# Kernel optimization log

Measured on AMD Instinct MI355X. Metric: run time of the kernel, lower is better.

Reference implementation:

```python
import jax, jax.numpy as jnp
import numpy as np

N_NODES = 400
HID = 96
DEC = 64
FEAT_STATIC = 8
FEAT = FEAT_STATIC + N_NODES  # 408
EPS = 1e-8


def prelu(x, a):
    # single-parameter PReLU (torch default num_parameters=1)
    return jnp.where(x >= 0, x, a * x)


def setup_inputs() -> dict:
    key = jax.random.key(0)
    ks = jax.random.split(key, 16)
    B = 16
    E = N_NODES * (N_NODES - 1) // 2  # 79800

    x = jax.random.normal(ks[0], (B, E), dtype=jnp.float32)
    node_features = jax.random.normal(ks[1], (B, N_NODES, FEAT_STATIC), dtype=jnp.float32)
    sc_matrix = jax.random.uniform(ks[2], (B, N_NODES, N_NODES), dtype=jnp.float32)

    # normalization buffers (computed from train split in torch; random stand-ins)
    static_mean = jax.random.normal(ks[3], (1, 1, FEAT_STATIC), dtype=jnp.float32) * 0.1
    static_std = jnp.ones((1, 1, FEAT_STATIC), dtype=jnp.float32)

    def lin(k, fin, fout):
        kw, kb = jax.random.split(k)
        lim = 1.0 / np.sqrt(fin)
        W = jax.random.uniform(kw, (fin, fout), minval=-lim, maxval=lim, dtype=jnp.float32)
        b = jax.random.uniform(kb, (fout,), minval=-lim, maxval=lim, dtype=jnp.float32)
        return W, b

    W_e1, b_e1 = lin(ks[4], FEAT, HID)
    W_e2, b_e2 = lin(ks[5], HID, HID)
    W_d1, b_d1 = lin(ks[6], 3 * HID, DEC)  # symmetric decoder: 3 * node_embed_dim
    W_d2, b_d2 = lin(ks[7], DEC, DEC)
    W_d3, b_d3 = lin(ks[8], DEC, 1)

    a25 = jnp.float32(0.25)

    ei_np, ej_np = np.triu_indices(N_NODES, k=1)
    ei = jnp.asarray(ei_np, dtype=jnp.int32)
    ej = jnp.asarray(ej_np, dtype=jnp.int32)

    return {
        "x": x, "node_features": node_features, "sc_matrix": sc_matrix,
        "static_mean": static_mean, "static_std": static_std,
        "W_e1": W_e1, "b_e1": b_e1, "a_e1": a25,
        "W_e2": W_e2, "b_e2": b_e2, "a_e2": a25,
        "W_d1": W_d1, "b_d1": b_d1, "a_d1": a25,
        "W_d2": W_d2, "b_d2": b_d2, "a_d2": a25,
        "W_d3": W_d3, "b_d3": b_d3,
        "ei": ei, "ej": ej,
    }


def reference(x, node_features, sc_matrix, static_mean, static_std,
              W_e1, b_e1, a_e1, W_e2, b_e2, a_e2,
              W_d1, b_d1, a_d1, W_d2, b_d2, a_d2, W_d3, b_d3, ei, ej):
    # x (SC upper triangle) is only used for batch size in the torch module.
    # static anatomical block: z-score with train stats
    s = (node_features - static_mean) / (static_std + EPS)  # [B,N,8]
    # sc_row block, 'brain_scale': divide by per-matrix mean
    m = sc_matrix / jnp.maximum(
        jnp.mean(sc_matrix, axis=(-2, -1), keepdims=True), EPS)  # [B,N,N]
    feats = jnp.concatenate([s, m], axis=-1)  # [B,N,408]

    # shared node encoder (dropout inactive at eval)
    h = prelu(feats @ W_e1 + b_e1, a_e1)
    h = prelu(h @ W_e2 + b_e2, a_e2)  # [B,N,96]

    # per-edge gather over upper-triangle indices
    h_i = h[:, ei, :]  # [B,E,96]
    h_j = h[:, ej, :]
    # symmetric edge features
    edge_feat = jnp.concatenate(
        [h_i + h_j, jnp.abs(h_i - h_j), h_i * h_j], axis=-1)  # [B,E,288]

    z = prelu(edge_feat @ W_d1 + b_d1, a_d1)
    z = prelu(z @ W_d2 + b_d2, a_d2)
    out = (z @ W_d3 + b_d3)[..., 0]  # [B,E]
    return out
```

## Files before the change

kernel.cpp:

```cpp
#include <hip/hip_runtime.h>

#define NN 400
#define HID 96
#define EDGES 79800
#define BATCH 16
#define ROWS (BATCH*EDGES)
#define NTILES 4988
#define NBLK 768

typedef _Float16 f16;
typedef f16 f16x2 __attribute__((ext_vector_type(2)));
typedef f16 f16x8 __attribute__((ext_vector_type(8)));
typedef __fp16 fp16x2 __attribute__((ext_vector_type(2)));
typedef float f32x16 __attribute__((ext_vector_type(16)));
typedef unsigned int u32;
typedef unsigned long long u64;

union H8 { f16x8 h; u32 u[4]; f16x2 p[4]; fp16x2 q[4]; u64 d[2]; };
union C2 { f16x2 h; fp16x2 q; u32 u; };

__device__ inline f16x2 pkrtz(float a, float b) {
  C2 c; c.q = __builtin_amdgcn_cvt_pkrtz(a, b); return c.h;
}
__device__ inline u32 pkrtz_u(float a, float b) {
  C2 c; c.q = __builtin_amdgcn_cvt_pkrtz(a, b); return c.u;
}
__device__ inline float fdot2a(f16x2 a, f16x2 b, float c) {
#if __has_builtin(__builtin_amdgcn_fdot2)
  C2 ca, cb; ca.h = a; cb.h = b;
  return __builtin_amdgcn_fdot2(ca.q, cb.q, c, false);
#else
  return c + (float)a.x*(float)b.x + (float)a.y*(float)b.y;
#endif
}

__device__ inline f16x8 habs8(f16x8 x) {
  H8 t; t.h = x;
  t.u[0] &= 0x7fff7fffu; t.u[1] &= 0x7fff7fffu;
  t.u[2] &= 0x7fff7fffu; t.u[3] &= 0x7fff7fffu;
  return t.h;
}

__device__ inline f16x8 pack8(float a0,float a1,float a2,float a3,
                              float a4,float a5,float a6,float a7){
  H8 u;
  u.p[0] = pkrtz(a0,a1);
  u.p[1] = pkrtz(a2,a3);
  u.p[2] = pkrtz(a4,a5);
  u.p[3] = pkrtz(a6,a7);
  return u.h;
}

__global__ void prep_mean_kernel(const float* __restrict__ We1, const float* __restrict__ We2,
                                 const float* __restrict__ W1, const float* __restrict__ W2,
                                 const float* __restrict__ sc,
                                 u32* __restrict__ wq, float* __restrict__ mpart) {
  if (blockIdx.x >= 140) {
    int p = blockIdx.x - 140;
    int b = p >> 2, part = p & 3;
    const float4* src = (const float4*)(sc + (size_t)b*160000) + part*10000;
    float s = 0.f;
    for (int i = threadIdx.x; i < 10000; i += 256) {
      float4 v = src[i];
      s += (v.x + v.y) + (v.z + v.w);
    }
    __shared__ float red[256];
    red[threadIdx.x] = s; __syncthreads();
    for (int off = 128; off > 0; off >>= 1) {
      if (threadIdx.x < off) red[threadIdx.x] += red[threadIdx.x + off];
      __syncthreads();
    }
    if (threadIdx.x == 0) mpart[p] = red[0];
    return;
  }
  int D = blockIdx.x*256 + threadIdx.x;
  float v0, v1;
  if (D < 9216) {
    int frag = D >> 8;  int t = frag >> 1, q = frag & 1;
    int rem = D & 255;  int lane = rem >> 2, dj = rem & 3;
    int c = lane & 31, h2 = lane >> 5;
    int k = 16*t + 8*h2 + 2*dj;
    int d = 32*q + c;
    v0 = W1[k*64 + d]; v1 = W1[(k+1)*64 + d];
  } else if (D < 11264) {
    int Dl = D - 9216;
    int frag = Dl >> 8; int t2 = frag >> 1, q = frag & 1;
    int rem = Dl & 255; int lane = rem >> 2, dj = rem & 3;
    int c = lane & 31, h2 = lane >> 5;
    int p = 8*t2 + 4*h2 + dj;
    int d = 32*q + c;
    v0 = W2[p*64 + d]; v1 = W2[(p+32)*64 + d];
  } else if (D < 31232) {
    int Dl = D - 11264;
    int frag = Dl >> 8; int t = frag/3, ct = frag - 3*t;
    int rem = Dl & 255; int lane = rem >> 2, dj = rem & 3;
    int c = lane & 31, h2 = lane >> 5;
    int k0 = 16*t + 8*h2 + 2*dj, k1 = k0 + 1;
    int d = 32*ct + c;
    v0 = (k0 < 400) ? We1[(8+k0)*96 + d] : (k0 < 408 ? We1[(k0-400)*96 + d] : 0.f);
    v1 = (k1 < 400) ? We1[(8+k1)*96 + d] : (k1 < 408 ? We1[(k1-400)*96 + d] : 0.f);
  } else {
    int Dl = D - 31232;
    int frag = Dl >> 8; int t = frag/3, ct = frag - 3*t;
    int rem = Dl & 255; int lane = rem >> 2, dj = rem & 3;
    int c = lane & 31, h2 = lane >> 5;
    int k = 16*t + 8*h2 + 2*dj;
    int p0 = (k   < 64) ? ((k&1)*32 + (k>>1))       : k;
    int p1 = (k+1 < 64) ? (((k+1)&1)*32 + ((k+1)>>1)) : (k+1);
    int d = 32*ct + c;
    v0 = We2[p0*96 + d]; v1 = We2[p1*96 + d];
  }
  wq[D] = pkrtz_u(v0, v1);
}

#define EST 210
__global__ __launch_bounds__(64) void enc_kernel(
    const float* __restrict__ sc, const float* __restrict__ nf,
    const float* __restrict__ smean, const float* __restrict__ sstd,
    const float* __restrict__ be1, const float* __restrict__ ae1,
    const float* __restrict__ be2, const float* __restrict__ ae2,
    const float* __restrict__ mpart, const u32* __restrict__ wq,
    f16* __restrict__ hout) {
  __shared__ u32 st[32*EST];
  const int lane = threadIdx.x;
  const int rt = blockIdx.x;
  const int r0 = rt*32;
  {
    int row = lane >> 1, half = lane & 1;
    int r = r0 + row;
    int b = r / 400;
    float ms = mpart[4*b] + mpart[4*b+1] + mpart[4*b+2] + mpart[4*b+3];
    float rm = 1.f / fmaxf(ms*(1.f/160000.f), 1e-8f);
    const float4* src = (const float4*)(sc + (size_t)r*400) + half*50;
    u32* dst = st + row*EST + half*100;
#pragma unroll 5
    for (int i = 0; i < 50; ++i) {
      float4 v = src[i];
      u32 lo = pkrtz_u(v.x*rm, v.y*rm);
      u32 hi = pkrtz_u(v.z*rm, v.w*rm);
      u64 w = (u64)lo | ((u64)hi << 32);
      *(u64*)(dst + 2*i) = w;
    }
  }
  const int c = lane & 31, h2 = lane >> 5;
  const float a1 = *ae1, a2 = *ae2;
  f32x16 acc[3];
#pragma unroll
  for (int q = 0; q < 3; ++q) {
    float bv = be1[32*q + c];
#pragma unroll
    for (int i = 0; i < 16; ++i) acc[q][i] = bv;
  }
  const u32* wb1 = wq + 11264;
#pragma unroll 5
  for (int t = 0; t < 25; ++t) {
    H8 av;
    const u32* ap = st + c*EST + 8*t + 4*h2;
    av.d[0] = *(const u64*)ap;
    av.d[1] = *(const u64*)(ap + 2);
#pragma unroll
    for (int ct = 0; ct < 3; ++ct) {
      f16x8 bf = *(const f16x8*)(wb1 + ((t*3+ct)*64 + lane)*4);
      acc[ct] = __builtin_amdgcn_mfma_f32_32x32x16_f16(av.h, bf, acc[ct], 0,0,0);
    }
  }
  {
    f16x8 af = {};
    if (h2 == 0) {
      int r = r0 + c;
      float q0[8];
#pragma unroll
      for (int j = 0; j < 8; ++j)
        q0[j] = (nf[r*8 + j] - smean[j]) / (sstd[j] + 1e-8f);
      af = pack8(q0[0],q0[1],q0[2],q0[3],q0[4],q0[5],q0[6],q0[7]);
    }
#pragma unroll
    for (int ct = 0; ct < 3; ++ct) {
      f16x8 bf = *(const f16x8*)(wb1 + ((25*3+ct)*64 + lane)*4);
      acc[ct] = __builtin_amdgcn_mfma_f32_32x32x16_f16(af, bf, acc[ct], 0,0,0);
    }
  }
  u32* zb = st;
#pragma unroll
  for (int r = 0; r < 16; ++r) {
    float x0 = acc[0][r]; x0 = fmaxf(x0, a1*x0);
    float x1 = acc[1][r]; x1 = fmaxf(x1, a1*x1);
    float x2 = acc[2][r]; x2 = fmaxf(x2, a1*x2);
    int row = (r & 3) + 8*(r >> 2) + 4*h2;
    zb[row*52 + c] = pkrtz_u(x0, x1);
    ((f16*)zb)[row*104 + 64 + c] = (f16)x2;
  }
  f32x16 acc2[3];
#pragma unroll
  for (int q = 0; q < 3; ++q) {
    float bv = be2[32*q + c];
#pragma unroll
    for (int i = 0; i < 16; ++i) acc2[q][i] = bv;
  }
  const u32* wb2 = wq + 31232;
#pragma unroll
  for (int t = 0; t < 6; ++t) {
    f16x8 af = *(const f16x8*)((const f16*)zb + c*104 + 16*t + 8*h2);
#pragma unroll
    for (int ct = 0; ct < 3; ++ct) {
      f16x8 bf = *(const f16x8*)(wb2 + ((t*3+ct)*64 + lane)*4);
      acc2[ct] = __builtin_amdgcn_mfma_f32_32x32x16_f16(af, bf, acc2[ct], 0,0,0);
    }
  }
#pragma unroll
  for (int ct = 0; ct < 3; ++ct)
#pragma unroll
    for (int rr = 0; rr < 16; ++rr) {
      int row = (rr & 3) + 8*(rr >> 2) + 4*h2;
      float v = acc2[ct][rr]; v = fmaxf(v, a2*v);
      hout[(r0 + row)*96 + 32*ct + c] = (f16)v;
    }
}

__global__ __launch_bounds__(256, 2) void decoder_kernel(
    const f16* __restrict__ hbuf, const u32* __restrict__ wq,
    const float* __restrict__ b1, const float* __restrict__ b2,
    const float* __restrict__ ad1, const float* __restrict__ ad2,
    const float* __restrict__ W3, const float* __restrict__ b3p,
    const int* __restrict__ ei, const int* __restrict__ ej,
    float* __restrict__ out) {
  __shared__ f16 wfr[17408];
  __shared__ u32 zbuf[4][1152];
  {
    float4* dst = (float4*)wfr;
    const float4* src = (const float4*)wq;
    for (int i = threadIdx.x; i < 2176; i += 256) dst[i] = src[i];
  }
  __syncthreads();
  const int lane = threadIdx.x & 63;
  const int wid  = threadIdx.x >> 6;
  const int c = lane & 31, h2 = lane >> 5;
  u32* zb = zbuf[wid];
  f16x8 bp5[2];
  bp5[0] = *(const f16x8*)(wq + ((34+0)*64 + lane)*4);
  bp5[1] = *(const f16x8*)(wq + ((34+1)*64 + lane)*4);
  f16x8 w2f[4][2];
#pragma unroll
  for (int t2 = 0; t2 < 4; ++t2) {
    w2f[t2][0] = *(const f16x8*)(wq + 9216 + ((t2*2+0)*64 + lane)*4);
    w2f[t2][1] = *(const f16x8*)(wq + 9216 + ((t2*2+1)*64 + lane)*4);
  }
  const float b1x = b1[c], b1y = b1[c+32];
  const float b2x = b2[c], b2y = b2[c+32];
  const float a1 = *ad1, a2 = *ad2, b3 = *b3p;
  const f16x2 a1v = pkrtz(a1, a1);
  const f16x2 a2v = pkrtz(a2, a2);
  const f16x2 w3p = pkrtz(W3[c], W3[c+32]);
  const f16x2 ones2 = pkrtz(1.f, 1.f);

  int tile = blockIdx.x;
  int nii[2], njj[2]; bool nvalid[2];
#pragma unroll
  for (int m = 0; m < 2; ++m) {
    int r = tile*256 + wid*64 + 32*m + c;
    nvalid[m] = (r < ROWS);
    unsigned rr = nvalid[m] ? (unsigned)r : (unsigned)(ROWS-1);
    unsigned bb = rr / (unsigned)EDGES;
    int e = (int)(rr - bb*(unsigned)EDGES);
    nii[m] = (int)(bb*NN) + ei[e];
    njj[m] = (int)(bb*NN) + ej[e];
  }

  for (; tile < NTILES; tile += NBLK) {
    const int rbase = tile*256 + wid*64;
    const f16* pi[2]; const f16* pj[2];
    bool valid[2];
#pragma unroll
    for (int m = 0; m < 2; ++m) {
      valid[m] = nvalid[m];
      pi[m] = hbuf + (nii[m]*HID + 8*h2);
      pj[m] = hbuf + (njj[m]*HID + 8*h2);
    }
    int ntile = tile + NBLK;
    if (ntile < NTILES) {
#pragma unroll
      for (int m = 0; m < 2; ++m) {
        int r = ntile*256 + wid*64 + 32*m + c;
        nvalid[m] = (r < ROWS);
        unsigned rr = nvalid[m] ? (unsigned)r : (unsigned)(ROWS-1);
        unsigned bb = rr / (unsigned)EDGES;
        int e = (int)(rr - bb*(unsigned)EDGES);
        nii[m] = (int)(bb*NN) + ei[e];
        njj[m] = (int)(bb*NN) + ej[e];
      }
    }
    f32x16 acc[2][2];
#pragma unroll
    for (int r = 0; r < 16; ++r) {
      acc[0][0][r] = b1x; acc[0][1][r] = b1y;
      acc[1][0][r] = b1x; acc[1][1][r] = b1y;
    }
#pragma unroll
    for (int t = 0; t < 6; ++t) {
      f16x8 bs0 = *(const f16x8*)(wfr + (((t   )*2+0)*64 + lane)*8);
      f16x8 bs1 = *(const f16x8*)(wfr + (((t   )*2+1)*64 + lane)*8);
      f16x8 bd0 = *(const f16x8*)(wfr + (((t+ 6)*2+0)*64 + lane)*8);
      f16x8 bd1 = *(const f16x8*)(wfr + (((t+ 6)*2+1)*64 + lane)*8);
      f16x8 bp0 = (t < 5) ? *(const f16x8*)(wfr + (((t+12)*2+0)*64 + lane)*8) : bp5[0];
      f16x8 bp1 = (t < 5) ? *(const f16x8*)(wfr + (((t+12)*2+1)*64 + lane)*8) : bp5[1];
#pragma unroll
      for (int m = 0; m < 2; ++m) {
        f16x8 hi = *(const f16x8*)(pi[m] + 16*t);
        f16x8 hj = *(const f16x8*)(pj[m] + 16*t);
        f16x8 su = hi + hj;
        f16x8 di = habs8(hi - hj);
        f16x8 pr = hi * hj;
        acc[m][0] = __builtin_amdgcn_mfma_f32_32x32x16_f16(su, bs0, acc[m][0], 0,0,0);
        acc[m][1] = __builtin_amdgcn_mfma_f32_32x32x16_f16(su, bs1, acc[m][1], 0,0,0);
        acc[m][0] = __builtin_amdgcn_mfma_f32_32x32x16_f16(di, bd0, acc[m][0], 0,0,0);
        acc[m][1] = __builtin_amdgcn_mfma_f32_32x32x16_f16(di, bd1, acc[m][1], 0,0,0);
        acc[m][0] = __builtin_amdgcn_mfma_f32_32x32x16_f16(pr, bp0, acc[m][0], 0,0,0);
        acc[m][1] = __builtin_amdgcn_mfma_f32_32x32x16_f16(pr, bp1, acc[m][1], 0,0,0);
      }
    }
#pragma unroll
    for (int m = 0; m < 2; ++m) {
#pragma unroll
      for (int r = 0; r < 16; ++r) {
        f16x2 p = pkrtz(acc[m][0][r], acc[m][1][r]);
        p = __builtin_elementwise_max(p, p * a1v);
        C2 cv; cv.h = p;
        int row = (r & 3) + 8*(r >> 2) + 4*h2;
        zb[row*36 + c] = cv.u;
      }
      f16x8 za[4];
#pragma unroll
      for (int t2 = 0; t2 < 4; ++t2)
        za[t2] = *(const f16x8*)((const f16*)zb + (c*36 + 8*t2 + 4*h2)*2);
      f32x16 zacc[2];
#pragma unroll
      for (int r = 0; r < 16; ++r) { zacc[0][r] = b2x; zacc[1][r] = b2y; }
#pragma unroll
      for (int t2 = 0; t2 < 4; ++t2) {
        zacc[0] = __builtin_amdgcn_mfma_f32_32x32x16_f16(za[t2], w2f[t2][0], zacc[0], 0,0,0);
        zacc[1] = __builtin_amdgcn_mfma_f32_32x32x16_f16(za[t2], w2f[t2][1], zacc[1], 0,0,0);
      }
#pragma unroll
      for (int r = 0; r < 16; ++r) {
        f16x2 p = pkrtz(zacc[0][r], zacc[1][r]);
        p = __builtin_elementwise_max(p, p * a2v);
        p = p * w3p;
        C2 cv; cv.h = p;
        int row = (r & 3) + 8*(r >> 2) + 4*h2;
        zb[row*36 + c] = cv.u;
      }
      float ssum = 0.f;
#pragma unroll
      for (int g = 0; g < 4; ++g) {
        H8 v; v.h = *(const f16x8*)((const f16*)zb + (c*36 + 16*h2 + 4*g)*2);
#pragma unroll
        for (int dw = 0; dw < 4; ++dw)
          ssum = fdot2a(v.p[dw], ones2, ssum);
      }
      ssum += __shfl_xor(ssum, 32);
      if (h2 == 0 && valid[m]) out[rbase + 32*m + c] = ssum + b3;
    }
  }
}

extern "C" void kernel_launch(void* const* d_in, const int* in_sizes, int n_in,
                              void* d_out, int out_size, void* d_ws, size_t ws_size,
                              hipStream_t stream) {
  const float* nf  = (const float*)d_in[1];
  const float* sc  = (const float*)d_in[2];
  const float* sm  = (const float*)d_in[3];
  const float* ss  = (const float*)d_in[4];
  const float* We1 = (const float*)d_in[5];
  const float* be1 = (const float*)d_in[6];
  const float* ae1 = (const float*)d_in[7];
  const float* We2 = (const float*)d_in[8];
  const float* be2 = (const float*)d_in[9];
  const float* ae2 = (const float*)d_in[10];
  const float* W1  = (const float*)d_in[11];
  const float* b1  = (const float*)d_in[12];
  const float* a1  = (const float*)d_in[13];
  const float* W2  = (const float*)d_in[14];
  const float* b2  = (const float*)d_in[15];
  const float* a2  = (const float*)d_in[16];
  const float* W3  = (const float*)d_in[17];
  const float* b3  = (const float*)d_in[18];
  const int*   ei  = (const int*)d_in[19];
  const int*   ej  = (const int*)d_in[20];
  float* out = (float*)d_out;

  char* ws = (char*)d_ws;
  float* mpart = (float*)ws;
  f16*   hbuf = (f16*)(ws + 256);
  u32*   wq   = (u32*)(ws + 256 + 1228800);

  prep_mean_kernel<<<204, 256, 0, stream>>>(We1, We2, W1, W2, sc, wq, mpart);
  enc_kernel<<<200, 64, 0, stream>>>(sc, nf, sm, ss, be1, ae1, be2, ae2,
                                     mpart, wq, hbuf);
  decoder_kernel<<<NBLK, 256, 0, stream>>>(hbuf, wq, b1, b2, a1, a2, W3, b3,
                                           ei, ej, out);
}
```

Measured before the change: 208.4 us.

## Split encoder K-loop across four waves, widen mean reduction, drop decoder LDS weights

The encoder now runs four waves per block. Each wave handles a slice of the first-layer K loop, and the partial accumulators are reduced through LDS before the second layer, which is split by output column tile across three waves. The sc mean reduction uses 16 parts per matrix instead of 4. The decoder no longer stages first-layer weights in LDS and reads them straight from global memory (cache). The decoder grid also grows from 768 to 1024 blocks. The aim is more parallelism in the small encoder and less LDS pressure and setup in the decoder. The cost is extra global/cache traffic for weight fragments in the decoder's inner loop and extra syncs in the encoder.

After: 212.6 us. 2.0% more time.

```diff
diff --git a/kernel.cpp b/kernel.cpp
--- a/kernel.cpp
+++ b/kernel.cpp
@@ -6,7 +6,7 @@
 #define BATCH 16
 #define ROWS (BATCH*EDGES)
 #define NTILES 4988
-#define NBLK 768
+#define NBLK 1024
 
 typedef _Float16 f16;
 typedef f16 f16x2 __attribute__((ext_vector_type(2)));
@@ -18,6 +18,7 @@
 
 union H8 { f16x8 h; u32 u[4]; f16x2 p[4]; fp16x2 q[4]; u64 d[2]; };
 union C2 { f16x2 h; fp16x2 q; u32 u; };
+union A16 { f32x16 v; float4 f[4]; };
 
 __device__ inline f16x2 pkrtz(float a, float b) {
   C2 c; c.q = __builtin_amdgcn_cvt_pkrtz(a, b); return c.h;
@@ -57,10 +58,10 @@
                                  u32* __restrict__ wq, float* __restrict__ mpart) {
   if (blockIdx.x >= 140) {
     int p = blockIdx.x - 140;
-    int b = p >> 2, part = p & 3;
-    const float4* src = (const float4*)(sc + (size_t)b*160000) + part*10000;
+    int b = p >> 4, part = p & 15;
+    const float4* src = (const float4*)(sc + (size_t)b*160000) + part*2500;
     float s = 0.f;
-    for (int i = threadIdx.x; i < 10000; i += 256) {
+    for (int i = threadIdx.x; i < 2500; i += 256) {
       float4 v = src[i];
       s += (v.x + v.y) + (v.z + v.w);
     }
@@ -105,116 +106,127 @@
     int rem = Dl & 255; int lane = rem >> 2, dj = rem & 3;
     int c = lane & 31, h2 = lane >> 5;
     int k = 16*t + 8*h2 + 2*dj;
-    int p0 = (k   < 64) ? ((k&1)*32 + (k>>1))       : k;
-    int p1 = (k+1 < 64) ? (((k+1)&1)*32 + ((k+1)>>1)) : (k+1);
     int d = 32*ct + c;
-    v0 = We2[p0*96 + d]; v1 = We2[p1*96 + d];
+    v0 = We2[k*96 + d]; v1 = We2[(k+1)*96 + d];
   }
   wq[D] = pkrtz_u(v0, v1);
 }
 
-#define EST 210
-__global__ __launch_bounds__(64) void enc_kernel(
+__global__ __launch_bounds__(256) void enc_kernel(
     const float* __restrict__ sc, const float* __restrict__ nf,
     const float* __restrict__ smean, const float* __restrict__ sstd,
     const float* __restrict__ be1, const float* __restrict__ ae1,
     const float* __restrict__ be2, const float* __restrict__ ae2,
     const float* __restrict__ mpart, const u32* __restrict__ wq,
     f16* __restrict__ hout) {
-  __shared__ u32 st[32*EST];
-  const int lane = threadIdx.x;
-  const int rt = blockIdx.x;
-  const int r0 = rt*32;
+  __shared__ u32 lds[12288 + 1664];
+  const int tid = threadIdx.x;
+  const int wid = tid >> 6, lane = tid & 63;
+  const int c = lane & 31, h2 = lane >> 5;
+  const int r0 = blockIdx.x * 32;
   {
-    int row = lane >> 1, half = lane & 1;
+    int row = tid >> 3, seg = tid & 7;
     int r = r0 + row;
     int b = r / 400;
-    float ms = mpart[4*b] + mpart[4*b+1] + mpart[4*b+2] + mpart[4*b+3];
+    float ms = 0.f;
+    const float4* mp4 = (const float4*)(mpart + 16*b);
+#pragma unroll
+    for (int k = 0; k < 4; ++k) { float4 v = mp4[k]; ms += (v.x+v.y)+(v.z+v.w); }
     float rm = 1.f / fmaxf(ms*(1.f/160000.f), 1e-8f);
-    const float4* src = (const float4*)(sc + (size_t)r*400) + half*50;
-    u32* dst = st + row*EST + half*100;
-#pragma unroll 5
-    for (int i = 0; i < 50; ++i) {
-      float4 v = src[i];
-      u32 lo = pkrtz_u(v.x*rm, v.y*rm);
-      u32 hi = pkrtz_u(v.z*rm, v.w*rm);
-      u64 w = (u64)lo | ((u64)hi << 32);
-      *(u64*)(dst + 2*i) = w;
-    }
-  }
-  const int c = lane & 31, h2 = lane >> 5;
-  const float a1 = *ae1, a2 = *ae2;
-  f32x16 acc[3];
-#pragma unroll
-  for (int q = 0; q < 3; ++q) {
-    float bv = be1[32*q + c];
-#pragma unroll
-    for (int i = 0; i < 16; ++i) acc[q][i] = bv;
-  }
+    const float4* src = (const float4*)(sc + (size_t)r*400);
+#pragma unroll
+    for (int i = 0; i < 13; ++i) {
+      int col4 = seg + 8*i;
+      if (col4 < 100) {
+        float4 v = src[col4];
+        u32 lo = pkrtz_u(v.x*rm, v.y*rm);
+        u32 hi = pkrtz_u(v.z*rm, v.w*rm);
+        *(u64*)(lds + row*210 + col4*2) = (u64)lo | ((u64)hi << 32);
+      }
+    }
+  }
+  __syncthreads();
+  int tb = (wid==0) ? 0 : (wid==1) ? 7 : (wid==2) ? 14 : 20;
+  int te = (wid==0) ? 7 : (wid==1) ? 14 : (wid==2) ? 20 : 26;
+  f32x16 acc[3] = {};
   const u32* wb1 = wq + 11264;
-#pragma unroll 5
-  for (int t = 0; t < 25; ++t) {
-    H8 av;
-    const u32* ap = st + c*EST + 8*t + 4*h2;
-    av.d[0] = *(const u64*)ap;
-    av.d[1] = *(const u64*)(ap + 2);
+  for (int t = tb; t < te; ++t) {
+    f16x8 af;
+    if (t < 25) {
+      H8 av;
+      const u32* ap = lds + c*210 + 8*t + 4*h2;
+      av.d[0] = *(const u64*)ap;
+      av.d[1] = *(const u64*)(ap + 2);
+      af = av.h;
+    } else {
+      af = (f16x8){};
+      if (h2 == 0) {
+        int r = r0 + c;
+        float q0[8];
+#pragma unroll
+        for (int j = 0; j < 8; ++j)
+          q0[j] = (nf[r*8 + j] - smean[j]) / (sstd[j] + 1e-8f);
+        af = pack8(q0[0],q0[1],q0[2],q0[3],q0[4],q0[5],q0[6],q0[7]);
+      }
+    }
 #pragma unroll
     for (int ct = 0; ct < 3; ++ct) {
       f16x8 bf = *(const f16x8*)(wb1 + ((t*3+ct)*64 + lane)*4);
-      acc[ct] = __builtin_amdgcn_mfma_f32_32x32x16_f16(av.h, bf, acc[ct], 0,0,0);
-    }
-  }
-  {
-    f16x8 af = {};
-    if (h2 == 0) {
-      int r = r0 + c;
-      float q0[8];
-#pragma unroll
-      for (int j = 0; j < 8; ++j)
-        q0[j] = (nf[r*8 + j] - smean[j]) / (sstd[j] + 1e-8f);
-      af = pack8(q0[0],q0[1],q0[2],q0[3],q0[4],q0[5],q0[6],q0[7]);
-    }
-#pragma unroll
-    for (int ct = 0; ct < 3; ++ct) {
-      f16x8 bf = *(const f16x8*)(wb1 + ((25*3+ct)*64 + lane)*4);
       acc[ct] = __builtin_amdgcn_mfma_f32_32x32x16_f16(af, bf, acc[ct], 0,0,0);
     }
   }
-  u32* zb = st;
-#pragma unroll
-  for (int r = 0; r < 16; ++r) {
-    float x0 = acc[0][r]; x0 = fmaxf(x0, a1*x0);
-    float x1 = acc[1][r]; x1 = fmaxf(x1, a1*x1);
-    float x2 = acc[2][r]; x2 = fmaxf(x2, a1*x2);
-    int row = (r & 3) + 8*(r >> 2) + 4*h2;
-    zb[row*52 + c] = pkrtz_u(x0, x1);
-    ((f16*)zb)[row*104 + 64 + c] = (f16)x2;
-  }
-  f32x16 acc2[3];
-#pragma unroll
-  for (int q = 0; q < 3; ++q) {
-    float bv = be2[32*q + c];
-#pragma unroll
-    for (int i = 0; i < 16; ++i) acc2[q][i] = bv;
-  }
-  const u32* wb2 = wq + 31232;
-#pragma unroll
-  for (int t = 0; t < 6; ++t) {
-    f16x8 af = *(const f16x8*)((const f16*)zb + c*104 + 16*t + 8*h2);
-#pragma unroll
-    for (int ct = 0; ct < 3; ++ct) {
-      f16x8 bf = *(const f16x8*)(wb2 + ((t*3+ct)*64 + lane)*4);
-      acc2[ct] = __builtin_amdgcn_mfma_f32_32x32x16_f16(af, bf, acc2[ct], 0,0,0);
-    }
-  }
-#pragma unroll
-  for (int ct = 0; ct < 3; ++ct)
+  __syncthreads();
+#pragma unroll
+  for (int ct = 0; ct < 3; ++ct) {
+    A16 u; u.v = acc[ct];
+#pragma unroll
+    for (int i4 = 0; i4 < 4; ++i4)
+      *(float4*)(lds + (((wid*3+ct)*4 + i4)*64 + lane)*4) = u.f[i4];
+  }
+  __syncthreads();
+  f16* zb16 = (f16*)(lds + 12288);
+  const float a1 = *ae1;
+  if (wid < 3) {
+    float bv = be1[32*wid + c];
+    f32x16 s;
+#pragma unroll
+    for (int i = 0; i < 16; ++i) s[i] = bv;
+#pragma unroll
+    for (int w2 = 0; w2 < 4; ++w2) {
+#pragma unroll
+      for (int i4 = 0; i4 < 4; ++i4) {
+        float4 f = *(const float4*)(lds + (((w2*3+wid)*4 + i4)*64 + lane)*4);
+        s[4*i4+0] += f.x; s[4*i4+1] += f.y; s[4*i4+2] += f.z; s[4*i4+3] += f.w;
+      }
+    }
+#pragma unroll
+    for (int r = 0; r < 16; ++r) {
+      float v = s[r]; v = fmaxf(v, a1*v);
+      int row = (r & 3) + 8*(r >> 2) + 4*h2;
+      zb16[row*104 + 32*wid + c] = (f16)v;
+    }
+  }
+  __syncthreads();
+  if (wid < 3) {
+    const float a2 = *ae2;
+    float bv = be2[32*wid + c];
+    f32x16 acc2;
+#pragma unroll
+    for (int i = 0; i < 16; ++i) acc2[i] = bv;
+    const u32* wb2 = wq + 31232;
+#pragma unroll
+    for (int t = 0; t < 6; ++t) {
+      f16x8 af = *(const f16x8*)(zb16 + c*104 + 16*t + 8*h2);
+      f16x8 bf = *(const f16x8*)(wb2 + ((t*3+wid)*64 + lane)*4);
+      acc2 = __builtin_amdgcn_mfma_f32_32x32x16_f16(af, bf, acc2, 0,0,0);
+    }
 #pragma unroll
     for (int rr = 0; rr < 16; ++rr) {
       int row = (rr & 3) + 8*(rr >> 2) + 4*h2;
-      float v = acc2[ct][rr]; v = fmaxf(v, a2*v);
-      hout[(r0 + row)*96 + 32*ct + c] = (f16)v;
-    }
+      float v = acc2[rr]; v = fmaxf(v, a2*v);
+      hout[(r0 + row)*96 + 32*wid + c] = (f16)v;
+    }
+  }
 }
 
 __global__ __launch_bounds__(256, 2) void decoder_kernel(
@@ -224,21 +236,11 @@
     const float* __restrict__ W3, const float* __restrict__ b3p,
     const int* __restrict__ ei, const int* __restrict__ ej,
     float* __restrict__ out) {
-  __shared__ f16 wfr[17408];
   __shared__ u32 zbuf[4][1152];
-  {
-    float4* dst = (float4*)wfr;
-    const float4* src = (const float4*)wq;
-    for (int i = threadIdx.x; i < 2176; i += 256) dst[i] = src[i];
-  }
-  __syncthreads();
   const int lane = threadIdx.x & 63;
   const int wid  = threadIdx.x >> 6;
   const int c = lane & 31, h2 = lane >> 5;
   u32* zb = zbuf[wid];
-  f16x8 bp5[2];
-  bp5[0] = *(const f16x8*)(wq + ((34+0)*64 + lane)*4);
-  bp5[1] = *(const f16x8*)(wq + ((34+1)*64 + lane)*4);
   f16x8 w2f[4][2];
 #pragma unroll
   for (int t2 = 0; t2 < 4; ++t2) {
@@ -267,6 +269,7 @@
   }
 
   for (; tile < NTILES; tile += NBLK) {
+    asm volatile("" ::: "memory");
     const int rbase = tile*256 + wid*64;
     const f16* pi[2]; const f16* pj[2];
     bool valid[2];
@@ -297,12 +300,12 @@
     }
 #pragma unroll
     for (int t = 0; t < 6; ++t) {
-      f16x8 bs0 = *(const f16x8*)(wfr + (((t   )*2+0)*64 + lane)*8);
-      f16x8 bs1 = *(const f16x8*)(wfr + (((t   )*2+1)*64 + lane)*8);
-      f16x8 bd0 = *(const f16x8*)(wfr + (((t+ 6)*2+0)*64 + lane)*8);
-      f16x8 bd1 = *(const f16x8*)(wfr + (((t+ 6)*2+1)*64 + lane)*8);
-      f16x8 bp0 = (t < 5) ? *(const f16x8*)(wfr + (((t+12)*2+0)*64 + lane)*8) : bp5[0];
-      f16x8 bp1 = (t < 5) ? *(const f16x8*)(wfr + (((t+12)*2+1)*64 + lane)*8) : bp5[1];
+      f16x8 bs0 = *(const f16x8*)(wq + (((t   )*2+0)*64 + lane)*4);
+      f16x8 bs1 = *(const f16x8*)(wq + (((t   )*2+1)*64 + lane)*4);
+      f16x8 bd0 = *(const f16x8*)(wq + (((t+ 6)*2+0)*64 + lane)*4);
+      f16x8 bd1 = *(const f16x8*)(wq + (((t+ 6)*2+1)*64 + lane)*4);
+      f16x8 bp0 = *(const f16x8*)(wq + (((t+12)*2+0)*64 + lane)*4);
+      f16x8 bp1 = *(const f16x8*)(wq + (((t+12)*2+1)*64 + lane)*4);
 #pragma unroll
       for (int m = 0; m < 2; ++m) {
         f16x8 hi = *(const f16x8*)(pi[m] + 16*t);
@@ -390,12 +393,12 @@
 
   char* ws = (char*)d_ws;
   float* mpart = (float*)ws;
-  f16*   hbuf = (f16*)(ws + 256);
-  u32*   wq   = (u32*)(ws + 256 + 1228800);
-
-  prep_mean_kernel<<<204, 256, 0, stream>>>(We1, We2, W1, W2, sc, wq, mpart);
-  enc_kernel<<<200, 64, 0, stream>>>(sc, nf, sm, ss, be1, ae1, be2, ae2,
-                                     mpart, wq, hbuf);
+  f16*   hbuf = (f16*)(ws + 1024);
+  u32*   wq   = (u32*)(ws + 1024 + 1228800);
+
+  prep_mean_kernel<<<396, 256, 0, stream>>>(We1, We2, W1, W2, sc, wq, mpart);
+  enc_kernel<<<200, 256, 0, stream>>>(sc, nf, sm, ss, be1, ae1, be2, ae2,
+                                      mpart, wq, hbuf);
   decoder_kernel<<<NBLK, 256, 0, stream>>>(hbuf, wq, b1, b2, a1, a2, W3, b3,
                                            ei, ej, out);
 }
```
